# Optimization experiments

Hardware: AMD Instinct MI355X
Metric: run time of the kernel (lower is better)

Reference implementation:

```python
import jax, jax.numpy as jnp
import numpy as np

N_NODES = 50000
N_GRAPHS = 50
MAX_NODES = 1000  # equal-size graphs
C_IN = 128
C_OUT = 128
N_EDGES = 800000
N_LAYERS = 3
BN_EPS = 1e-5


def setup_inputs() -> dict:
    key = jax.random.key(0)
    ks = jax.random.split(key, 20)
    x = jax.random.normal(ks[0], (N_NODES, C_IN), dtype=jnp.float32)
    edge_index = jax.random.randint(ks[1], (2, N_EDGES), 0, N_NODES, dtype=jnp.int64)
    batch = jnp.repeat(jnp.arange(N_GRAPHS, dtype=jnp.int64), MAX_NODES)
    s_in = 1.0 / np.sqrt(C_IN)
    s_out = 1.0 / np.sqrt(C_OUT)
    fh_W = jax.random.normal(ks[2], (C_IN, C_OUT), dtype=jnp.float32) * s_in
    fh_b = jnp.zeros((C_OUT,), dtype=jnp.float32)
    W1 = jax.random.normal(ks[3], (N_LAYERS, C_OUT, C_OUT), dtype=jnp.float32) * s_out
    b1 = jnp.zeros((N_LAYERS, C_OUT), dtype=jnp.float32)
    g1 = jnp.ones((N_LAYERS, C_OUT), dtype=jnp.float32)
    be1 = jnp.zeros((N_LAYERS, C_OUT), dtype=jnp.float32)
    W2 = jax.random.normal(ks[4], (N_LAYERS, C_OUT, C_OUT), dtype=jnp.float32) * s_out
    b2 = jnp.zeros((N_LAYERS, C_OUT), dtype=jnp.float32)
    g2 = jnp.ones((N_LAYERS, C_OUT), dtype=jnp.float32)
    be2 = jnp.zeros((N_LAYERS, C_OUT), dtype=jnp.float32)
    return {"x": x, "edge_index": edge_index, "batch": batch,
            "fh_W": fh_W, "fh_b": fh_b,
            "W1": W1, "b1": b1, "g1": g1, "be1": be1,
            "W2": W2, "b2": b2, "g2": g2, "be2": be2}


def _bn(h, gamma, beta):
    # training-mode BatchNorm1d over the node dim (biased variance, like torch)
    mu = jnp.mean(h, axis=0)
    var = jnp.var(h, axis=0)
    return (h - mu) * jax.lax.rsqrt(var + BN_EPS) * gamma + beta


def _mlp(h, W1, b1, g1, be1, W2, b2, g2, be2):
    h = jax.nn.relu(_bn(h @ W1 + b1, g1, be1))
    h = jax.nn.relu(_bn(h @ W2 + b2, g2, be2))
    return h


def _to_dense_batch(h, batch):
    # counts per graph -> exclusive starts -> intra-graph position
    ones = jnp.ones((h.shape[0],), dtype=jnp.int32)
    counts = jax.ops.segment_sum(ones, batch, num_segments=N_GRAPHS)
    starts = jnp.cumsum(counts) - counts
    pos = jnp.arange(h.shape[0], dtype=jnp.int32) - starts[batch]
    dense = jnp.zeros((N_GRAPHS, MAX_NODES, h.shape[1]), dtype=h.dtype)
    return dense.at[batch, pos].set(h)


def reference(x, edge_index, batch, fh_W, fh_b, W1, b1, g1, be1, W2, b2, g2, be2):
    src, dst = edge_index[0], edge_index[1]
    h = x @ fh_W + fh_b  # first_head Linear
    outs = [_to_dense_batch(h, batch)]
    for l in range(N_LAYERS):
        # GINConv: mlp((1+eps)*x + sum_{j->i} x_j), eps=0
        agg = jax.ops.segment_sum(h[src], dst, num_segments=N_NODES)
        h = _mlp(h + agg, W1[l], b1[l], g1[l], be1[l], W2[l], b2[l], g2[l], be2[l])
        outs.append(_to_dense_batch(h, batch))
    return jnp.stack(outs)  # [N_LAYERS+1, B, MAX_NODES, C]
```

## Files before the change

### kernel.cpp

```cpp
#include <hip/hip_runtime.h>

#define NN 50000
#define NE 800000
#define CC 128
#define SLAB (NN * CC)
#define BN_EPS 1e-5f

typedef __attribute__((ext_vector_type(8))) short bf16x8;
typedef __attribute__((ext_vector_type(4))) float f32x4;
typedef unsigned short ushort_t;
typedef unsigned int uint_t;

__device__ inline ushort_t f2bf(float v) {
  unsigned u = __builtin_bit_cast(unsigned, v);
  unsigned r = u + 0x7FFFu + ((u >> 16) & 1u);
  return (ushort_t)(r >> 16);
}
__device__ inline float bf2f(unsigned lo16) { return __builtin_bit_cast(float, lo16 << 16); }

__global__ void zero_int_kernel(int* __restrict__ p, int n) {
  int i = blockIdx.x * blockDim.x + threadIdx.x;
  if (i < n) p[i] = 0;
}

__global__ void count_kernel(const int* __restrict__ dst, int* __restrict__ counts) {
  int e = blockIdx.x * blockDim.x + threadIdx.x;
  if (e < NE) atomicAdd(&counts[dst[e]], 1);
}

__global__ void scan1_kernel(const int* __restrict__ counts, int* __restrict__ excl,
                             int* __restrict__ blocksum) {
  __shared__ int s[256];
  int t = threadIdx.x;
  int i = blockIdx.x * 256 + t;
  int v = (i < NN) ? counts[i] : 0;
  s[t] = v;
  for (int off = 1; off < 256; off <<= 1) {
    __syncthreads();
    int add = (t >= off) ? s[t - off] : 0;
    __syncthreads();
    s[t] += add;
  }
  __syncthreads();
  if (i < NN) excl[i] = s[t] - v;
  if (t == 255) blocksum[blockIdx.x] = s[255];
}

__global__ void scan2_kernel(int* __restrict__ blocksum, int nb) {
  __shared__ int s[256];
  int t = threadIdx.x;
  int v = (t < nb) ? blocksum[t] : 0;
  s[t] = v;
  for (int off = 1; off < 256; off <<= 1) {
    __syncthreads();
    int add = (t >= off) ? s[t - off] : 0;
    __syncthreads();
    s[t] += add;
  }
  __syncthreads();
  if (t < nb) blocksum[t] = s[t] - v;
}

__global__ void scan3_kernel(int* __restrict__ excl, const int* __restrict__ blocksum) {
  int i = blockIdx.x * 256 + threadIdx.x;
  if (i < NN) excl[i] += blocksum[blockIdx.x];
}

__global__ void fill_kernel(const int* __restrict__ src, const int* __restrict__ dst,
                            const int* __restrict__ starts, int* __restrict__ fill,
                            int* __restrict__ bucket) {
  int e = blockIdx.x * blockDim.x + threadIdx.x;
  if (e < NE) {
    int d = dst[e];
    int pos = atomicAdd(&fill[d], 1);
    bucket[starts[d] + pos] = src[e];
  }
}

__global__ void prep_w_kernel(const float* __restrict__ fh_W, const float* __restrict__ W1,
                              const float* __restrict__ W2, short* __restrict__ whi,
                              short* __restrict__ wlo) {
  int m = blockIdx.x;
  const float* src = (m == 0) ? fh_W : ((m <= 3) ? W1 + (m - 1) * CC * CC : W2 + (m - 4) * CC * CC);
  short* hi = whi + m * CC * CC;
  short* lo = wlo + m * CC * CC;
  for (int it = 0; it < 64; ++it) {
    int idx = it * 256 + threadIdx.x;
    int j = idx & 7;
    int l = (idx >> 3) & 63;
    int nt = (idx >> 9) & 7;
    int ks = idx >> 12;
    int n = nt * 16 + (l & 15);
    int k = ks * 32 + ((l >> 4) << 3) + j;
    float v = src[k * CC + n];
    unsigned u = __builtin_bit_cast(unsigned, v);
    unsigned short h = (unsigned short)(u >> 16);
    float hf = __builtin_bit_cast(float, ((unsigned)h) << 16);
    float r = v - hf;
    unsigned ur = __builtin_bit_cast(unsigned, r);
    hi[idx] = (short)h;
    lo[idx] = (short)(ur >> 16);
  }
}

__global__ __launch_bounds__(256) void gemm0_kernel(
    const float* __restrict__ A, const short* __restrict__ Wp_hi, const short* __restrict__ Wp_lo,
    const float* __restrict__ bias, float* __restrict__ out, ushort_t* __restrict__ h16s) {
  const int t = threadIdx.x;
  const int l = t & 63;
  const int wv = t >> 6;
  const int m0 = blockIdx.x * 64 + wv * 16;
  const int row = m0 + (l & 15);
  const int kg = (l >> 4) * 8;

  f32x4 acc[8];
#pragma unroll
  for (int i = 0; i < 8; ++i) acc[i] = (f32x4){0.f, 0.f, 0.f, 0.f};

#pragma unroll
  for (int ks = 0; ks < 4; ++ks) {
    float av[8];
    if (row < NN) {
      const float* ap = &A[row * CC + ks * 32 + kg];
      float4 v0 = *(const float4*)ap;
      float4 v1 = *(const float4*)(ap + 4);
      av[0] = v0.x; av[1] = v0.y; av[2] = v0.z; av[3] = v0.w;
      av[4] = v1.x; av[5] = v1.y; av[6] = v1.z; av[7] = v1.w;
    } else {
#pragma unroll
      for (int i = 0; i < 8; ++i) av[i] = 0.f;
    }
    bf16x8 ah, al;
#pragma unroll
    for (int i = 0; i < 8; ++i) {
      unsigned u = __builtin_bit_cast(unsigned, av[i]);
      unsigned short hbits = (unsigned short)(u >> 16);
      float hf = __builtin_bit_cast(float, ((unsigned)hbits) << 16);
      float r = av[i] - hf;
      unsigned ur = __builtin_bit_cast(unsigned, r);
      ah[i] = (short)hbits;
      al[i] = (short)(ur >> 16);
    }
#pragma unroll
    for (int nt = 0; nt < 8; ++nt) {
      const int base = (ks * 8 + nt) * 512 + l * 8;
      bf16x8 wh = *(const bf16x8*)&Wp_hi[base];
      bf16x8 wl = *(const bf16x8*)&Wp_lo[base];
      acc[nt] = __builtin_amdgcn_mfma_f32_16x16x32_bf16(ah, wh, acc[nt], 0, 0, 0);
      acc[nt] = __builtin_amdgcn_mfma_f32_16x16x32_bf16(al, wh, acc[nt], 0, 0, 0);
      acc[nt] = __builtin_amdgcn_mfma_f32_16x16x32_bf16(ah, wl, acc[nt], 0, 0, 0);
    }
  }

  const int rbase = m0 + (l >> 4) * 4;
  const int cn = l & 15;
#pragma unroll
  for (int nt = 0; nt < 8; ++nt) {
    int c = nt * 16 + cn;
    float bv = bias[c];
#pragma unroll
    for (int r = 0; r < 4; ++r) {
      int rr = rbase + r;
      if (rr < NN) {
        float v = acc[nt][r] + bv;
        out[rr * CC + c] = v;
        h16s[((c >> 5) * NN + rr) * 32 + (c & 31)] = f2bf(v);
      }
    }
  }
}

__global__ __launch_bounds__(256) void gather_kernel(
    const ushort_t* __restrict__ h16s, const int* __restrict__ starts,
    const int* __restrict__ counts, const int* __restrict__ bucket,
    ushort_t* __restrict__ aggs) {
  const int slice = blockIdx.x & 3;
  const int t = threadIdx.x;
  const int w = t >> 6;
  const int l = t & 63;
  const int q = l >> 4;
  const int j16 = l & 15;
  const int node = (blockIdx.x >> 2) * 4 + w;
  const uint_t* tbl = (const uint_t*)h16s + slice * (NN * 16);

  float a0 = 0.f, a1 = 0.f;
  if (q == 0) {
    uint_t u = tbl[node * 16 + j16];
    a0 = bf2f(u & 0xFFFFu);
    a1 = bf2f(u >> 16);
  }
  const int s = starts[node];
  const int n = counts[node];
  for (int base = 0; base < n; base += 64) {
    int nb = min(n - base, 64);
    int idx = (l < nb) ? bucket[s + base + l] : 0;
    int jj = 0;
    for (; jj + 32 <= nb; jj += 32) {
      int sr[8];
      uint_t u[8];
#pragma unroll
      for (int k = 0; k < 8; ++k) sr[k] = __shfl(idx, jj + 4 * k + q);
#pragma unroll
      for (int k = 0; k < 8; ++k) u[k] = tbl[sr[k] * 16 + j16];
#pragma unroll
      for (int k = 0; k < 8; ++k) {
        a0 += bf2f(u[k] & 0xFFFFu);
        a1 += bf2f(u[k] >> 16);
      }
    }
    for (; jj + 16 <= nb; jj += 16) {
      int sr[4];
      uint_t u[4];
#pragma unroll
      for (int k = 0; k < 4; ++k) sr[k] = __shfl(idx, jj + 4 * k + q);
#pragma unroll
      for (int k = 0; k < 4; ++k) u[k] = tbl[sr[k] * 16 + j16];
#pragma unroll
      for (int k = 0; k < 4; ++k) {
        a0 += bf2f(u[k] & 0xFFFFu);
        a1 += bf2f(u[k] >> 16);
      }
    }
    for (; jj < nb; jj += 4) {
      int i = jj + q;
      int sr = __shfl(idx, (i < nb) ? i : (nb - 1));
      if (i < nb) {
        uint_t u = tbl[sr * 16 + j16];
        a0 += bf2f(u & 0xFFFFu);
        a1 += bf2f(u >> 16);
      }
    }
  }
  a0 += __shfl_xor(a0, 16);
  a0 += __shfl_xor(a0, 32);
  a1 += __shfl_xor(a1, 16);
  a1 += __shfl_xor(a1, 32);
  if (q == 0) {
    ((uint_t*)aggs)[slice * (NN * 16) + node * 16 + j16] =
        (uint_t)f2bf(a0) | ((uint_t)f2bf(a1) << 16);
  }
}

__global__ __launch_bounds__(256) void gemm1_kernel(
    const ushort_t* __restrict__ aggs, const short* __restrict__ Wp_hi,
    const short* __restrict__ Wp_lo, const float* __restrict__ bias,
    ushort_t* __restrict__ tmp16, float* __restrict__ stats_out) {
  __shared__ float sred[2 * CC];
  const int t = threadIdx.x;
  const int l = t & 63;
  const int wv = t >> 6;
  const int m0 = blockIdx.x * 64 + wv * 16;
  const int row = m0 + (l & 15);
  const int kg = (l >> 4) * 8;
  sred[t] = 0.f;

  f32x4 acc[8];
#pragma unroll
  for (int i = 0; i < 8; ++i) acc[i] = (f32x4){0.f, 0.f, 0.f, 0.f};

#pragma unroll
  for (int ks = 0; ks < 4; ++ks) {
    bf16x8 ah;
    if (row < NN) {
      ah = *(const bf16x8*)&aggs[(ks * NN + row) * 32 + kg];
    } else {
#pragma unroll
      for (int i = 0; i < 8; ++i) ah[i] = 0;
    }
#pragma unroll
    for (int nt = 0; nt < 8; ++nt) {
      const int base = (ks * 8 + nt) * 512 + l * 8;
      bf16x8 wh = *(const bf16x8*)&Wp_hi[base];
      bf16x8 wl = *(const bf16x8*)&Wp_lo[base];
      acc[nt] = __builtin_amdgcn_mfma_f32_16x16x32_bf16(ah, wh, acc[nt], 0, 0, 0);
      acc[nt] = __builtin_amdgcn_mfma_f32_16x16x32_bf16(ah, wl, acc[nt], 0, 0, 0);
    }
  }

  __syncthreads();
  const int rbase = m0 + (l >> 4) * 4;
  const int cn = l & 15;
#pragma unroll
  for (int nt = 0; nt < 8; ++nt) {
    int c = nt * 16 + cn;
    float bv = bias[c];
    float s = 0.f, qq = 0.f;
#pragma unroll
    for (int r = 0; r < 4; ++r) {
      int rr = rbase + r;
      if (rr < NN) {
        float v = acc[nt][r] + bv;
        tmp16[rr * CC + c] = f2bf(v);
        s += v; qq += v * v;
      }
    }
    s += __shfl_xor(s, 16); s += __shfl_xor(s, 32);
    qq += __shfl_xor(qq, 16); qq += __shfl_xor(qq, 32);
    if ((l >> 4) == 0) {
      atomicAdd(&sred[c], s);
      atomicAdd(&sred[CC + c], qq);
    }
  }
  __syncthreads();
  atomicAdd(&stats_out[t], sred[t]);
}

__global__ __launch_bounds__(256) void gemm2_kernel(
    ushort_t* __restrict__ tmp16, const short* __restrict__ Wp_hi,
    const short* __restrict__ Wp_lo, const float* __restrict__ bias,
    const float* __restrict__ stats_in, const float* __restrict__ g,
    const float* __restrict__ be, float* __restrict__ stats_out) {
  __shared__ float sred[2 * CC];
  const int t = threadIdx.x;
  const int l = t & 63;
  const int wv = t >> 6;
  const int m0 = blockIdx.x * 64 + wv * 16;
  const int row = m0 + (l & 15);
  const int kg = (l >> 4) * 8;
  sred[t] = 0.f;

  f32x4 acc[8];
#pragma unroll
  for (int i = 0; i < 8; ++i) acc[i] = (f32x4){0.f, 0.f, 0.f, 0.f};

#pragma unroll
  for (int ks = 0; ks < 4; ++ks) {
    bf16x8 ah;
    if (row < NN) {
      bf16x8 raw = *(const bf16x8*)&tmp16[row * CC + ks * 32 + kg];
#pragma unroll
      for (int i = 0; i < 8; ++i) {
        int c = ks * 32 + kg + i;
        float mu = stats_in[c] * (1.0f / NN);
        float var = fmaxf(stats_in[CC + c] * (1.0f / NN) - mu * mu, 0.f);
        float a = g[c] * rsqrtf(var + BN_EPS);
        float d = fmaf(-mu, a, be[c]);
        float v = bf2f((unsigned)(ushort_t)raw[i]);
        v = fmaxf(fmaf(v, a, d), 0.f);
        ah[i] = (short)f2bf(v);
      }
    } else {
#pragma unroll
      for (int i = 0; i < 8; ++i) ah[i] = 0;
    }
#pragma unroll
    for (int nt = 0; nt < 8; ++nt) {
      const int base = (ks * 8 + nt) * 512 + l * 8;
      bf16x8 wh = *(const bf16x8*)&Wp_hi[base];
      bf16x8 wl = *(const bf16x8*)&Wp_lo[base];
      acc[nt] = __builtin_amdgcn_mfma_f32_16x16x32_bf16(ah, wh, acc[nt], 0, 0, 0);
      acc[nt] = __builtin_amdgcn_mfma_f32_16x16x32_bf16(ah, wl, acc[nt], 0, 0, 0);
    }
  }

  __syncthreads();
  const int rbase = m0 + (l >> 4) * 4;
  const int cn = l & 15;
#pragma unroll
  for (int nt = 0; nt < 8; ++nt) {
    int c = nt * 16 + cn;
    float bv = bias[c];
    float s = 0.f, qq = 0.f;
#pragma unroll
    for (int r = 0; r < 4; ++r) {
      int rr = rbase + r;
      if (rr < NN) {
        float v = acc[nt][r] + bv;
        tmp16[rr * CC + c] = f2bf(v);
        s += v; qq += v * v;
      }
    }
    s += __shfl_xor(s, 16); s += __shfl_xor(s, 32);
    qq += __shfl_xor(qq, 16); qq += __shfl_xor(qq, 32);
    if ((l >> 4) == 0) {
      atomicAdd(&sred[c], s);
      atomicAdd(&sred[CC + c], qq);
    }
  }
  __syncthreads();
  atomicAdd(&stats_out[t], sred[t]);
}

__global__ __launch_bounds__(256) void apply_kernel(
    const ushort_t* __restrict__ t2, const float* __restrict__ stats2,
    const float* __restrict__ g2, const float* __restrict__ be2,
    float* __restrict__ outslab, ushort_t* __restrict__ h16s) {
  const int node = blockIdx.x * 256 + threadIdx.x;
  const int slice = blockIdx.y;
  if (node >= NN) return;
  const int c0 = slice * 32;

  const uint4* tp = (const uint4*)(t2 + node * CC + c0);
  uint4 r[4];
#pragma unroll
  for (int i = 0; i < 4; ++i) r[i] = tp[i];

  float vo[32];
#pragma unroll
  for (int i = 0; i < 4; ++i) {
    unsigned ws[4] = {r[i].x, r[i].y, r[i].z, r[i].w};
#pragma unroll
    for (int j = 0; j < 4; ++j) {
      vo[i * 8 + 2 * j] = bf2f(ws[j] & 0xFFFFu);
      vo[i * 8 + 2 * j + 1] = bf2f(ws[j] >> 16);
    }
  }
#pragma unroll
  for (int j = 0; j < 32; ++j) {
    int c = c0 + j;
    float mu = stats2[c] * (1.0f / NN);
    float var = fmaxf(stats2[CC + c] * (1.0f / NN) - mu * mu, 0.f);
    float a = g2[c] * rsqrtf(var + BN_EPS);
    float d = fmaf(-mu, a, be2[c]);
    vo[j] = fmaxf(fmaf(vo[j], a, d), 0.f);
  }
  float* op = &outslab[node * CC + c0];
#pragma unroll
  for (int j = 0; j < 8; ++j) {
    float4 v = make_float4(vo[4 * j], vo[4 * j + 1], vo[4 * j + 2], vo[4 * j + 3]);
    *(float4*)&op[4 * j] = v;
  }
  if (h16s) {
    uint4* hp = (uint4*)(h16s + (slice * NN + node) * 32);
#pragma unroll
    for (int i = 0; i < 4; ++i) {
      uint4 o;
      o.x = (unsigned)f2bf(vo[i * 8 + 0]) | ((unsigned)f2bf(vo[i * 8 + 1]) << 16);
      o.y = (unsigned)f2bf(vo[i * 8 + 2]) | ((unsigned)f2bf(vo[i * 8 + 3]) << 16);
      o.z = (unsigned)f2bf(vo[i * 8 + 4]) | ((unsigned)f2bf(vo[i * 8 + 5]) << 16);
      o.w = (unsigned)f2bf(vo[i * 8 + 6]) | ((unsigned)f2bf(vo[i * 8 + 7]) << 16);
      hp[i] = o;
    }
  }
}

extern "C" void kernel_launch(void* const* d_in, const int* in_sizes, int n_in,
                              void* d_out, int out_size, void* d_ws, size_t ws_size,
                              hipStream_t stream) {
  const float* x    = (const float*)d_in[0];
  const int*   edge = (const int*)d_in[1];
  const float* fh_W = (const float*)d_in[3];
  const float* fh_b = (const float*)d_in[4];
  const float* W1   = (const float*)d_in[5];
  const float* b1   = (const float*)d_in[6];
  const float* g1   = (const float*)d_in[7];
  const float* be1  = (const float*)d_in[8];
  const float* W2   = (const float*)d_in[9];
  const float* b2   = (const float*)d_in[10];
  const float* g2   = (const float*)d_in[11];
  const float* be2  = (const float*)d_in[12];
  float* out = (float*)d_out;

  const int* src = edge;
  const int* dst = edge + NE;

  int* counts   = (int*)d_ws;
  int* fill     = counts + 50048;
  float* stats  = (float*)(fill + 50048);
  int* starts   = (int*)(stats + 1536);
  int* blocksum = starts + 50048;
  int* bucket   = blocksum + 256;
  short* whi    = (short*)(bucket + NE);
  short* wlo    = whi + 7 * CC * CC;
  ushort_t* h16s = (ushort_t*)(wlo + 7 * CC * CC);
  ushort_t* aggs = h16s + SLAB;
  ushort_t* tmp16 = aggs + SLAB;

  zero_int_kernel<<<(101632 + 255) / 256, 256, 0, stream>>>(counts, 101632);
  count_kernel<<<NE / 256, 256, 0, stream>>>(dst, counts);
  scan1_kernel<<<196, 256, 0, stream>>>(counts, starts, blocksum);
  scan2_kernel<<<1, 256, 0, stream>>>(blocksum, 196);
  scan3_kernel<<<196, 256, 0, stream>>>(starts, blocksum);
  fill_kernel<<<NE / 256, 256, 0, stream>>>(src, dst, starts, fill, bucket);

  prep_w_kernel<<<7, 256, 0, stream>>>(fh_W, W1, W2, whi, wlo);

  gemm0_kernel<<<782, 256, 0, stream>>>(x, whi, wlo, fh_b, out, h16s);

  for (int ly = 0; ly < 3; ++ly) {
    float* stats1 = stats + (ly * 2) * 256;
    float* stats2 = stats + (ly * 2 + 1) * 256;
    gather_kernel<<<50000, 256, 0, stream>>>(h16s, starts, counts, bucket, aggs);
    gemm1_kernel<<<782, 256, 0, stream>>>(
        aggs, whi + (1 + ly) * CC * CC, wlo + (1 + ly) * CC * CC, b1 + ly * CC, tmp16, stats1);
    gemm2_kernel<<<782, 256, 0, stream>>>(
        tmp16, whi + (4 + ly) * CC * CC, wlo + (4 + ly) * CC * CC, b2 + ly * CC,
        stats1, g1 + ly * CC, be1 + ly * CC, stats2);
    apply_kernel<<<dim3(196, 4), 256, 0, stream>>>(
        tmp16, stats2, g2 + ly * CC, be2 + ly * CC, out + (ly + 1) * SLAB,
        (ly < 2) ? h16s : (ushort_t*)nullptr);
  }
}
```

Before: 596.0 us.

## Switch bf16 features to row-major layout; gather full rows per wave

Replaces the four-slice channel-split bf16 layout of the node features and aggregates with a plain row-major [node][128] layout. The gather kernel now handles all 128 channels of a node in one wave, each lane loading 8 bytes of a 256-byte row, so it issues a quarter as many blocks and reads each neighbour index once instead of four times. The apply kernel precomputes the BN scale and shift into shared memory once per block and maps four threads to one node's channel quarters. The trade-off is larger per-row gather transactions and the loss of the per-slice locality the old layout gave in L2.

```diff
diff --git a/kernel.cpp b/kernel.cpp
--- a/kernel.cpp
+++ b/kernel.cpp
@@ -105,7 +105,7 @@
 
 __global__ __launch_bounds__(256) void gemm0_kernel(
     const float* __restrict__ A, const short* __restrict__ Wp_hi, const short* __restrict__ Wp_lo,
-    const float* __restrict__ bias, float* __restrict__ out, ushort_t* __restrict__ h16s) {
+    const float* __restrict__ bias, float* __restrict__ out, ushort_t* __restrict__ h16) {
   const int t = threadIdx.x;
   const int l = t & 63;
   const int wv = t >> 6;
@@ -164,85 +164,106 @@
       if (rr < NN) {
         float v = acc[nt][r] + bv;
         out[rr * CC + c] = v;
-        h16s[((c >> 5) * NN + rr) * 32 + (c & 31)] = f2bf(v);
+        h16[rr * CC + c] = f2bf(v);
       }
     }
   }
 }
 
 __global__ __launch_bounds__(256) void gather_kernel(
-    const ushort_t* __restrict__ h16s, const int* __restrict__ starts,
+    const ushort_t* __restrict__ h16, const int* __restrict__ starts,
     const int* __restrict__ counts, const int* __restrict__ bucket,
-    ushort_t* __restrict__ aggs) {
-  const int slice = blockIdx.x & 3;
+    ushort_t* __restrict__ agg16) {
   const int t = threadIdx.x;
-  const int w = t >> 6;
+  const int node = blockIdx.x * 4 + (t >> 6);
   const int l = t & 63;
-  const int q = l >> 4;
-  const int j16 = l & 15;
-  const int node = (blockIdx.x >> 2) * 4 + w;
-  const uint_t* tbl = (const uint_t*)h16s + slice * (NN * 16);
-
-  float a0 = 0.f, a1 = 0.f;
-  if (q == 0) {
-    uint_t u = tbl[node * 16 + j16];
-    a0 = bf2f(u & 0xFFFFu);
-    a1 = bf2f(u >> 16);
-  }
+  const int h = l >> 5;
+  const int j8 = l & 31;
+  const uint2* tbl = (const uint2*)h16;
+
+  float a0, a1, a2, a3;
+  if (h == 0) {
+    uint2 u = tbl[node * 32 + j8];
+    a0 = bf2f(u.x & 0xFFFFu); a1 = bf2f(u.x >> 16);
+    a2 = bf2f(u.y & 0xFFFFu); a3 = bf2f(u.y >> 16);
+  } else {
+    a0 = a1 = a2 = a3 = 0.f;
+  }
+
   const int s = starts[node];
   const int n = counts[node];
   for (int base = 0; base < n; base += 64) {
-    int nb = min(n - base, 64);
-    int idx = (l < nb) ? bucket[s + base + l] : 0;
+    const int nb = min(n - base, 64);
+    const int idx = (l < nb) ? bucket[s + base + l] : 0;
     int jj = 0;
-    for (; jj + 32 <= nb; jj += 32) {
+    for (; jj + 16 <= nb; jj += 16) {
       int sr[8];
-      uint_t u[8];
-#pragma unroll
-      for (int k = 0; k < 8; ++k) sr[k] = __shfl(idx, jj + 4 * k + q);
-#pragma unroll
-      for (int k = 0; k < 8; ++k) u[k] = tbl[sr[k] * 16 + j16];
+#pragma unroll
+      for (int k = 0; k < 8; ++k) sr[k] = __shfl(idx, jj + 2 * k + h);
+      uint2 u[8];
+#pragma unroll
+      for (int k = 0; k < 8; ++k) u[k] = tbl[sr[k] * 32 + j8];
 #pragma unroll
       for (int k = 0; k < 8; ++k) {
-        a0 += bf2f(u[k] & 0xFFFFu);
-        a1 += bf2f(u[k] >> 16);
-      }
-    }
-    for (; jj + 16 <= nb; jj += 16) {
+        a0 += bf2f(u[k].x & 0xFFFFu); a1 += bf2f(u[k].x >> 16);
+        a2 += bf2f(u[k].y & 0xFFFFu); a3 += bf2f(u[k].y >> 16);
+      }
+    }
+    if (jj + 8 <= nb) {
       int sr[4];
-      uint_t u[4];
-#pragma unroll
-      for (int k = 0; k < 4; ++k) sr[k] = __shfl(idx, jj + 4 * k + q);
-#pragma unroll
-      for (int k = 0; k < 4; ++k) u[k] = tbl[sr[k] * 16 + j16];
+#pragma unroll
+      for (int k = 0; k < 4; ++k) sr[k] = __shfl(idx, jj + 2 * k + h);
+      uint2 u[4];
+#pragma unroll
+      for (int k = 0; k < 4; ++k) u[k] = tbl[sr[k] * 32 + j8];
 #pragma unroll
       for (int k = 0; k < 4; ++k) {
-        a0 += bf2f(u[k] & 0xFFFFu);
-        a1 += bf2f(u[k] >> 16);
-      }
-    }
-    for (; jj < nb; jj += 4) {
-      int i = jj + q;
-      int sr = __shfl(idx, (i < nb) ? i : (nb - 1));
-      if (i < nb) {
-        uint_t u = tbl[sr * 16 + j16];
-        a0 += bf2f(u & 0xFFFFu);
-        a1 += bf2f(u >> 16);
-      }
-    }
-  }
-  a0 += __shfl_xor(a0, 16);
+        a0 += bf2f(u[k].x & 0xFFFFu); a1 += bf2f(u[k].x >> 16);
+        a2 += bf2f(u[k].y & 0xFFFFu); a3 += bf2f(u[k].y >> 16);
+      }
+      jj += 8;
+    }
+    if (jj + 4 <= nb) {
+      int sr0 = __shfl(idx, jj + h);
+      int sr1 = __shfl(idx, jj + 2 + h);
+      uint2 u0 = tbl[sr0 * 32 + j8];
+      uint2 u1 = tbl[sr1 * 32 + j8];
+      a0 += bf2f(u0.x & 0xFFFFu) + bf2f(u1.x & 0xFFFFu);
+      a1 += bf2f(u0.x >> 16) + bf2f(u1.x >> 16);
+      a2 += bf2f(u0.y & 0xFFFFu) + bf2f(u1.y & 0xFFFFu);
+      a3 += bf2f(u0.y >> 16) + bf2f(u1.y >> 16);
+      jj += 4;
+    }
+    if (jj + 2 <= nb) {
+      int sr = __shfl(idx, jj + h);
+      uint2 u = tbl[sr * 32 + j8];
+      a0 += bf2f(u.x & 0xFFFFu); a1 += bf2f(u.x >> 16);
+      a2 += bf2f(u.y & 0xFFFFu); a3 += bf2f(u.y >> 16);
+      jj += 2;
+    }
+    if (jj < nb) {
+      int sr = __shfl(idx, jj);
+      if (h == 0) {
+        uint2 u = tbl[sr * 32 + j8];
+        a0 += bf2f(u.x & 0xFFFFu); a1 += bf2f(u.x >> 16);
+        a2 += bf2f(u.y & 0xFFFFu); a3 += bf2f(u.y >> 16);
+      }
+    }
+  }
   a0 += __shfl_xor(a0, 32);
-  a1 += __shfl_xor(a1, 16);
   a1 += __shfl_xor(a1, 32);
-  if (q == 0) {
-    ((uint_t*)aggs)[slice * (NN * 16) + node * 16 + j16] =
-        (uint_t)f2bf(a0) | ((uint_t)f2bf(a1) << 16);
+  a2 += __shfl_xor(a2, 32);
+  a3 += __shfl_xor(a3, 32);
+  if (h == 0) {
+    uint2 o;
+    o.x = (uint_t)f2bf(a0) | ((uint_t)f2bf(a1) << 16);
+    o.y = (uint_t)f2bf(a2) | ((uint_t)f2bf(a3) << 16);
+    ((uint2*)agg16)[node * 32 + j8] = o;
   }
 }
 
 __global__ __launch_bounds__(256) void gemm1_kernel(
-    const ushort_t* __restrict__ aggs, const short* __restrict__ Wp_hi,
+    const ushort_t* __restrict__ agg16, const short* __restrict__ Wp_hi,
     const short* __restrict__ Wp_lo, const float* __restrict__ bias,
     ushort_t* __restrict__ tmp16, float* __restrict__ stats_out) {
   __shared__ float sred[2 * CC];
@@ -262,7 +283,7 @@
   for (int ks = 0; ks < 4; ++ks) {
     bf16x8 ah;
     if (row < NN) {
-      ah = *(const bf16x8*)&aggs[(ks * NN + row) * 32 + kg];
+      ah = *(const bf16x8*)&agg16[row * CC + ks * 32 + kg];
     } else {
 #pragma unroll
       for (int i = 0; i < 8; ++i) ah[i] = 0;
@@ -384,11 +405,22 @@
 __global__ __launch_bounds__(256) void apply_kernel(
     const ushort_t* __restrict__ t2, const float* __restrict__ stats2,
     const float* __restrict__ g2, const float* __restrict__ be2,
-    float* __restrict__ outslab, ushort_t* __restrict__ h16s) {
-  const int node = blockIdx.x * 256 + threadIdx.x;
-  const int slice = blockIdx.y;
+    float* __restrict__ outslab, ushort_t* __restrict__ h16) {
+  __shared__ float bn[2 * CC];
+  const int t = threadIdx.x;
+  if (t < CC) {
+    float mu = stats2[t] * (1.0f / NN);
+    float var = fmaxf(stats2[CC + t] * (1.0f / NN) - mu * mu, 0.f);
+    float a = g2[t] * rsqrtf(var + BN_EPS);
+    bn[t] = a;
+    bn[CC + t] = fmaf(-mu, a, be2[t]);
+  }
+  __syncthreads();
+
+  const int idx = blockIdx.x * 256 + t;
+  const int node = idx >> 2;
   if (node >= NN) return;
-  const int c0 = slice * 32;
+  const int c0 = (idx & 3) * 32;
 
   const uint4* tp = (const uint4*)(t2 + node * CC + c0);
   uint4 r[4];
@@ -408,11 +440,7 @@
 #pragma unroll
   for (int j = 0; j < 32; ++j) {
     int c = c0 + j;
-    float mu = stats2[c] * (1.0f / NN);
-    float var = fmaxf(stats2[CC + c] * (1.0f / NN) - mu * mu, 0.f);
-    float a = g2[c] * rsqrtf(var + BN_EPS);
-    float d = fmaf(-mu, a, be2[c]);
-    vo[j] = fmaxf(fmaf(vo[j], a, d), 0.f);
+    vo[j] = fmaxf(fmaf(vo[j], bn[c], bn[CC + c]), 0.f);
   }
   float* op = &outslab[node * CC + c0];
 #pragma unroll
@@ -420,8 +448,8 @@
     float4 v = make_float4(vo[4 * j], vo[4 * j + 1], vo[4 * j + 2], vo[4 * j + 3]);
     *(float4*)&op[4 * j] = v;
   }
-  if (h16s) {
-    uint4* hp = (uint4*)(h16s + (slice * NN + node) * 32);
+  if (h16) {
+    uint4* hp = (uint4*)(h16 + node * CC + c0);
 #pragma unroll
     for (int i = 0; i < 4; ++i) {
       uint4 o;
@@ -462,9 +490,9 @@
   int* bucket   = blocksum + 256;
   short* whi    = (short*)(bucket + NE);
   short* wlo    = whi + 7 * CC * CC;
-  ushort_t* h16s = (ushort_t*)(wlo + 7 * CC * CC);
-  ushort_t* aggs = h16s + SLAB;
-  ushort_t* tmp16 = aggs + SLAB;
+  ushort_t* h16 = (ushort_t*)(wlo + 7 * CC * CC);
+  ushort_t* agg16 = h16 + SLAB;
+  ushort_t* tmp16 = agg16 + SLAB;
 
   zero_int_kernel<<<(101632 + 255) / 256, 256, 0, stream>>>(counts, 101632);
   count_kernel<<<NE / 256, 256, 0, stream>>>(dst, counts);
@@ -475,19 +503,19 @@
 
   prep_w_kernel<<<7, 256, 0, stream>>>(fh_W, W1, W2, whi, wlo);
 
-  gemm0_kernel<<<782, 256, 0, stream>>>(x, whi, wlo, fh_b, out, h16s);
+  gemm0_kernel<<<782, 256, 0, stream>>>(x, whi, wlo, fh_b, out, h16);
 
   for (int ly = 0; ly < 3; ++ly) {
     float* stats1 = stats + (ly * 2) * 256;
     float* stats2 = stats + (ly * 2 + 1) * 256;
-    gather_kernel<<<50000, 256, 0, stream>>>(h16s, starts, counts, bucket, aggs);
+    gather_kernel<<<NN / 4, 256, 0, stream>>>(h16, starts, counts, bucket, agg16);
     gemm1_kernel<<<782, 256, 0, stream>>>(
-        aggs, whi + (1 + ly) * CC * CC, wlo + (1 + ly) * CC * CC, b1 + ly * CC, tmp16, stats1);
+        agg16, whi + (1 + ly) * CC * CC, wlo + (1 + ly) * CC * CC, b1 + ly * CC, tmp16, stats1);
     gemm2_kernel<<<782, 256, 0, stream>>>(
         tmp16, whi + (4 + ly) * CC * CC, wlo + (4 + ly) * CC * CC, b2 + ly * CC,
         stats1, g1 + ly * CC, be1 + ly * CC, stats2);
-    apply_kernel<<<dim3(196, 4), 256, 0, stream>>>(
+    apply_kernel<<<782, 256, 0, stream>>>(
         tmp16, stats2, g2 + ly * CC, be2 + ly * CC, out + (ly + 1) * SLAB,
-        (ly < 2) ? h16s : (ushort_t*)nullptr);
-  }
-}
+        (ly < 2) ? h16 : (ushort_t*)nullptr);
+  }
+}
```

New measurement: 483.7 us. -18.8%, faster.
